# Performance work log

Measured on AMD Instinct MI355X. Metric: run time of the kernel, lower is better.

## Reference

```python
import jax, jax.numpy as jnp
import numpy as np

N_EMBD = 384
N_HEADS = 6
HEAD_SIZE = N_EMBD // N_HEADS  # 64
D_FF = 4 * N_EMBD
EPS = 1e-5


def layernorm(x, g, b):
    mu = jnp.mean(x, axis=-1, keepdims=True)
    var = jnp.var(x, axis=-1, keepdims=True)
    return (x - mu) * jax.lax.rsqrt(var + EPS) * g + b


def setup_inputs() -> dict:
    key = jax.random.key(0)
    ks = jax.random.split(key, 12)
    B, T, C, H, HS = 64, 256, N_EMBD, N_HEADS, HEAD_SIZE
    s = 0.02
    return {
        "x": jax.random.normal(ks[0], (B, T, C), jnp.float32),
        "Wq": jax.random.normal(ks[1], (H, C, HS), jnp.float32) * s,
        "Wk": jax.random.normal(ks[2], (H, C, HS), jnp.float32) * s,
        "Wv": jax.random.normal(ks[3], (H, C, HS), jnp.float32) * s,
        "Wo": jax.random.normal(ks[4], (C, C), jnp.float32) * s,
        "bo": jnp.zeros((C,), jnp.float32),
        "W1": jax.random.normal(ks[5], (C, D_FF), jnp.float32) * s,
        "b1": jnp.zeros((D_FF,), jnp.float32),
        "W2": jax.random.normal(ks[6], (D_FF, C), jnp.float32) * s,
        "b2": jnp.zeros((C,), jnp.float32),
        "g1": jnp.ones((C,), jnp.float32),
        "beta1": jnp.zeros((C,), jnp.float32),
        "g2": jnp.ones((C,), jnp.float32),
        "beta2": jnp.zeros((C,), jnp.float32),
    }


def reference(x, Wq, Wk, Wv, Wo, bo, W1, b1, W2, b2, g1, beta1, g2, beta2):
    B, T, C = x.shape
    # --- attention branch (dropout = identity in eval) ---
    h = layernorm(x, g1, beta1)
    q = jnp.einsum('btc,hck->bhtk', h, Wq)
    k = jnp.einsum('btc,hck->bhtk', h, Wk)
    v = jnp.einsum('btc,hck->bhtk', h, Wv)
    scale = HEAD_SIZE ** -0.5
    wei = jnp.einsum('bhtk,bhsk->bhts', q, k) * scale  # [B,H,T,T]
    causal = jnp.tril(jnp.ones((T, T), bool))
    wei = jnp.where(causal, wei, -jnp.inf)
    wei = jax.nn.softmax(wei, axis=-1)
    attn = jnp.einsum('bhts,bhsk->bthk', wei, v).reshape(B, T, C)
    x = x + attn @ Wo + bo
    # --- MLP branch ---
    h2 = layernorm(x, g2, beta2)
    ff = jax.nn.relu(h2 @ W1 + b1) @ W2 + b2
    return x + ff
```

## Files before the change

kernel.cpp:

```cpp
#include <hip/hip_runtime.h>

#define B 64
#define T 256
#define C 384
#define H 6
#define HS 64
#define DFF 1536
#define BT (B*T)

typedef __attribute__((ext_vector_type(8))) short short8;
typedef __attribute__((ext_vector_type(4))) float float4v;
typedef __attribute__((ext_vector_type(4))) unsigned short ushort4v;

static __device__ __forceinline__ unsigned short f2bf(float f) {
  unsigned int u = __float_as_uint(f);
  unsigned int r = (u + 0x7fffu + ((u >> 16) & 1u)) >> 16;
  return (unsigned short)r;
}

typedef __attribute__((address_space(1))) const unsigned int ga_u32;
typedef __attribute__((address_space(3))) unsigned int ls_u32;
static __device__ __forceinline__ void gld16(const void* g, void* l) {
  __builtin_amdgcn_global_load_lds((ga_u32*)g, (ls_u32*)l, 16, 0, 0);
}

__global__ __launch_bounds__(256) void prep_w(
    const float* __restrict__ Wq, const float* __restrict__ Wk, const float* __restrict__ Wv,
    const float* __restrict__ Wo, const float* __restrict__ W1, const float* __restrict__ W2,
    unsigned short* __restrict__ wqkv, unsigned short* __restrict__ wo,
    unsigned short* __restrict__ w1t, unsigned short* __restrict__ w2t) {
  __shared__ float tile[32][33];
  int bx = blockIdx.x;
  int x = threadIdx.x & 31, y = threadIdx.x >> 5;
  if (bx < 432) {
    int tn = bx % 36, tc = bx / 36;
    int n0 = tn * 32, c0 = tc * 32;
    int mat = n0 / 384, rem = n0 % 384, head = rem / 64, hs0 = rem % 64;
    const float* W = (mat == 0) ? Wq : ((mat == 1) ? Wk : Wv);
    const float* src = W + (size_t)head * C * HS + hs0;
    #pragma unroll
    for (int i = 0; i < 4; ++i) tile[y + 8 * i][x] = src[(size_t)(c0 + y + 8 * i) * 64 + x];
    __syncthreads();
    #pragma unroll
    for (int i = 0; i < 4; ++i)
      wqkv[(size_t)(n0 + y + 8 * i) * 384 + c0 + x] = f2bf(tile[x][y + 8 * i]);
    return;
  }
  const float* src; unsigned short* dst; int CN, R, n0, c0;
  if (bx < 576) {
    int t = bx - 432; n0 = (t % 12) * 32; c0 = (t / 12) * 32;
    src = Wo; dst = wo; CN = 384; R = 384;
  } else if (bx < 1152) {
    int t = bx - 576; n0 = (t % 48) * 32; c0 = (t / 48) * 32;
    src = W1; dst = w1t; CN = 1536; R = 384;
  } else {
    int t = bx - 1152; n0 = (t % 12) * 32; c0 = (t / 12) * 32;
    src = W2; dst = w2t; CN = 384; R = 1536;
  }
  #pragma unroll
  for (int i = 0; i < 4; ++i) tile[y + 8 * i][x] = src[(size_t)(c0 + y + 8 * i) * CN + n0 + x];
  __syncthreads();
  #pragma unroll
  for (int i = 0; i < 4; ++i)
    dst[(size_t)(n0 + y + 8 * i) * R + c0 + x] = f2bf(tile[x][y + 8 * i]);
}

__global__ __launch_bounds__(256) void ln_kernel(const float* __restrict__ x,
    const float* __restrict__ g, const float* __restrict__ bta,
    unsigned short* __restrict__ out) {
  int t = blockIdx.x * 4 + (threadIdx.x >> 6);
  int lane = threadIdx.x & 63;
  const float* row = x + (size_t)t * C;
  float v[6];
  float s = 0.f, ss = 0.f;
  #pragma unroll
  for (int i = 0; i < 6; ++i) {
    v[i] = row[lane + i * 64];
    s += v[i];
    ss += v[i] * v[i];
  }
  #pragma unroll
  for (int m = 32; m >= 1; m >>= 1) {
    s += __shfl_xor(s, m);
    ss += __shfl_xor(ss, m);
  }
  float mu = s / C;
  float var = ss / C - mu * mu;
  float rstd = rsqrtf(var + 1e-5f);
  unsigned short* orow = out + (size_t)t * C;
  #pragma unroll
  for (int i = 0; i < 6; ++i) {
    int c = lane + i * 64;
    orow[c] = f2bf((v[i] - mu) * rstd * g[c] + bta[c]);
  }
}

template<int EPI, int MT>
__global__ __launch_bounds__(MT >= 256 ? 512 : 256) void gemm_kernel(
    const unsigned short* __restrict__ A, const unsigned short* __restrict__ Wt,
    const float* __restrict__ bias, const float* __restrict__ resid,
    float* __restrict__ outf,
    unsigned short* __restrict__ outb, unsigned short* __restrict__ outb2,
    unsigned short* __restrict__ outb3, int K, int N) {
  __shared__ unsigned short Ash[MT * 64];
  __shared__ unsigned short Bsh[128 * 64];
  constexpr int NW = (MT >= 256) ? 8 : 4;
  constexpr int WM = NW / 2;
  constexpr int MR = MT / WM / 16;
  constexpr int NA = (MT / 8) / NW;
  constexpr int NB = 16 / NW;
  int tid = threadIdx.x, lane = tid & 63, w = tid >> 6;
  int wm = w >> 1, wn = w & 1;
  int bxs = ((blockIdx.x & 7) * (gridDim.x >> 3)) + (blockIdx.x >> 3);
  int m0 = bxs * MT, n0 = blockIdx.y * 128;
  int lrow = lane >> 3;
  int lchunk = (lane & 7) ^ (lrow & 7);
  int frow = lane & 15, cg = lane >> 4;
  float4v acc[MR][4] = {};
  for (int k0 = 0; k0 < K; k0 += 64) {
    __syncthreads();
    #pragma unroll
    for (int i = 0; i < NA; ++i) {
      int win = w * NA + i;
      gld16(A + (size_t)(m0 + win * 8 + lrow) * K + k0 + lchunk * 8, &Ash[win * 512]);
    }
    #pragma unroll
    for (int i = 0; i < NB; ++i) {
      int win = w * NB + i;
      gld16(Wt + (size_t)(n0 + win * 8 + lrow) * K + k0 + lchunk * 8, &Bsh[win * 512]);
    }
    __syncthreads();
    #pragma unroll
    for (int ks = 0; ks < 2; ++ks) {
      short8 af[MR], bf[4];
      #pragma unroll
      for (int mi = 0; mi < MR; ++mi) {
        int r = wm * (MR * 16) + mi * 16 + frow;
        int ch = (ks * 4 + cg) ^ (r & 7);
        af[mi] = *(const short8*)((const char*)Ash + r * 128 + ch * 16);
      }
      #pragma unroll
      for (int ni = 0; ni < 4; ++ni) {
        int r = wn * 64 + ni * 16 + frow;
        int ch = (ks * 4 + cg) ^ (r & 7);
        bf[ni] = *(const short8*)((const char*)Bsh + r * 128 + ch * 16);
      }
      #pragma unroll
      for (int mi = 0; mi < MR; ++mi)
        #pragma unroll
        for (int ni = 0; ni < 4; ++ni)
          acc[mi][ni] = __builtin_amdgcn_mfma_f32_16x16x32_bf16(af[mi], bf[ni], acc[mi][ni], 0, 0, 0);
    }
  }
  int cl = lane & 15;
  #pragma unroll
  for (int mi = 0; mi < MR; ++mi) {
    #pragma unroll
    for (int ni = 0; ni < 4; ++ni) {
      if constexpr (EPI == 0) {
        int gc = n0 + wn * 64 + ni * 16 + cl;
        int mat = gc / 384;
        int head = (gc % 384) >> 6;
        int hs = gc & 63;
        int gr0 = m0 + wm * (MR * 16) + mi * 16 + cg * 4;
        int tt0 = gr0 & 255, bidx = gr0 >> 8;
        size_t bhb = (size_t)(bidx * H + head);
        if (mat == 2) {
          ushort4v pk;
          #pragma unroll
          for (int j = 0; j < 4; ++j) pk[j] = f2bf(acc[mi][ni][j]);
          *(ushort4v*)&outb3[(bhb * HS + hs) * T + tt0] = pk;
        } else {
          unsigned short* dst = (mat == 0) ? outb : outb2;
          #pragma unroll
          for (int j = 0; j < 4; ++j)
            dst[(bhb * T + tt0 + j) * HS + hs] = f2bf(acc[mi][ni][j]);
        }
      } else {
        #pragma unroll
        for (int j = 0; j < 4; ++j) {
          int gr = m0 + wm * (MR * 16) + mi * 16 + cg * 4 + j;
          int gc = n0 + wn * 64 + ni * 16 + cl;
          float val = acc[mi][ni][j];
          if constexpr (EPI == 2) {
            outb[(size_t)gr * N + gc] = f2bf(fmaxf(val + bias[gc], 0.f));
          } else {
            size_t i = (size_t)gr * N + gc;
            outf[i] = resid[i] + val + bias[gc];
          }
        }
      }
    }
  }
}

__global__ __launch_bounds__(512) void proj_ln_kernel(
    const unsigned short* __restrict__ A, const unsigned short* __restrict__ Wt,
    const float* __restrict__ bo, const float* __restrict__ x,
    const float* __restrict__ g2, const float* __restrict__ be2,
    float* __restrict__ x2, unsigned short* __restrict__ h2) {
  __shared__ unsigned short Ash[64 * 64];
  __shared__ unsigned short Bsh[384 * 64];
  __shared__ float red[64][2][2];
  int tid = threadIdx.x, lane = tid & 63, w = tid >> 6;
  int wm = w >> 1, wn = w & 1;
  int bxs = ((blockIdx.x & 7) * (gridDim.x >> 3)) + (blockIdx.x >> 3);
  int m0 = bxs * 64;
  int lrow = lane >> 3;
  int lchunk = (lane & 7) ^ (lrow & 7);
  int frow = lane & 15, cg = lane >> 4, cl = lane & 15;
  float4v acc[12] = {};
  for (int k0 = 0; k0 < 384; k0 += 64) {
    __syncthreads();
    gld16(A + (size_t)(m0 + w * 8 + lrow) * 384 + k0 + lchunk * 8, &Ash[w * 512]);
    #pragma unroll
    for (int i = 0; i < 6; ++i) {
      int win = w * 6 + i;
      gld16(Wt + (size_t)(win * 8 + lrow) * 384 + k0 + lchunk * 8, &Bsh[win * 512]);
    }
    __syncthreads();
    #pragma unroll
    for (int ks = 0; ks < 2; ++ks) {
      int ra = wm * 16 + frow;
      int cha = (ks * 4 + cg) ^ (ra & 7);
      short8 af = *(const short8*)((const char*)Ash + ra * 128 + cha * 16);
      #pragma unroll
      for (int nt = 0; nt < 12; ++nt) {
        int rb = wn * 192 + nt * 16 + frow;
        int chb = (ks * 4 + cg) ^ (rb & 7);
        short8 bf = *(const short8*)((const char*)Bsh + rb * 128 + chb * 16);
        acc[nt] = __builtin_amdgcn_mfma_f32_16x16x32_bf16(af, bf, acc[nt], 0, 0, 0);
      }
    }
  }
  #pragma unroll
  for (int nt = 0; nt < 12; ++nt) {
    int gc = wn * 192 + nt * 16 + cl;
    #pragma unroll
    for (int j = 0; j < 4; ++j) {
      int gr = m0 + wm * 16 + cg * 4 + j;
      acc[nt][j] += x[(size_t)gr * 384 + gc] + bo[gc];
    }
  }
  __syncthreads();
  #pragma unroll
  for (int j = 0; j < 4; ++j) {
    float s = 0.f, ss = 0.f;
    #pragma unroll
    for (int nt = 0; nt < 12; ++nt) { float v = acc[nt][j]; s += v; ss += v * v; }
    #pragma unroll
    for (int off = 1; off < 16; off <<= 1) { s += __shfl_xor(s, off); ss += __shfl_xor(ss, off); }
    if (cl == 0) {
      int lr = wm * 16 + cg * 4 + j;
      red[lr][wn][0] = s;
      red[lr][wn][1] = ss;
    }
  }
  __syncthreads();
  #pragma unroll
  for (int j = 0; j < 4; ++j) {
    int lr = wm * 16 + cg * 4 + j;
    int gr = m0 + lr;
    float s = red[lr][0][0] + red[lr][1][0];
    float ss = red[lr][0][1] + red[lr][1][1];
    float mu = s / 384.f;
    float var = ss / 384.f - mu * mu;
    float rstd = rsqrtf(var + 1e-5f);
    #pragma unroll
    for (int nt = 0; nt < 12; ++nt) {
      int gc = wn * 192 + nt * 16 + cl;
      float v = acc[nt][j];
      x2[(size_t)gr * 384 + gc] = v;
      h2[(size_t)gr * 384 + gc] = f2bf((v - mu) * rstd * g2[gc] + be2[gc]);
    }
  }
}

__global__ __launch_bounds__(256) void attn_kernel(
    const unsigned short* __restrict__ qg, const unsigned short* __restrict__ kg,
    const unsigned short* __restrict__ vtg, unsigned short* __restrict__ ab) {
  __shared__ unsigned short Ksh[64 * 64];
  __shared__ unsigned short Vsh[64 * 256];
  __shared__ unsigned short Psh[4 * 16 * 256];
  int bh = blockIdx.x;
  int bb = bh / H, hh = bh % H;
  int qt = blockIdx.y, q0 = qt * 64;
  int tid = threadIdx.x, lane = tid & 63, w = tid >> 6;
  int cl = lane & 15, cg = lane >> 4;
  const float scale_log2e = 0.125f * 1.44269504f;
  const unsigned short* qp = qg + ((size_t)bh * T) * HS;
  const unsigned short* kp = kg + ((size_t)bh * T) * HS;
  const unsigned short* vp = vtg + ((size_t)bh * HS) * T;

  short8 aq[2];
  #pragma unroll
  for (int k0 = 0; k0 < 2; ++k0)
    aq[k0] = *(const short8*)&qp[(size_t)(q0 + w * 16 + cl) * HS + cg * 8 + k0 * 32];

  #pragma unroll
  for (int i = 0; i < 8; ++i) {
    int idx = tid + i * 256;
    int r = idx >> 5, c16 = idx & 31;
    uint4 val = *(const uint4*)&vp[(size_t)r * T + c16 * 8];
    int byte = (r * 512 + c16 * 16) ^ ((r & 7) << 4);
    *(uint4*)((char*)Vsh + byte) = val;
  }

  float4v sacc[4][4] = {};
  for (int si = 0; si <= qt; ++si) {
    __syncthreads();
    #pragma unroll
    for (int i = 0; i < 2; ++i) {
      int idx = tid + i * 256;
      int r = idx >> 3, c16 = idx & 7;
      uint4 val = *(const uint4*)&kp[(size_t)(si * 64 + r) * HS + c16 * 8];
      int byte = (r * 128 + c16 * 16) ^ ((r & 7) << 4);
      *(uint4*)((char*)Ksh + byte) = val;
    }
    __syncthreads();
    #pragma unroll
    for (int ss = 0; ss < 4; ++ss) {
      if (ss == si) {
        #pragma unroll
        for (int nt = 0; nt < 4; ++nt) {
          int srow = nt * 16 + cl;
          #pragma unroll
          for (int k0 = 0; k0 < 2; ++k0) {
            int byte = (srow * 128 + (cg * 8 + k0 * 32) * 2) ^ ((srow & 7) << 4);
            short8 bf = *(const short8*)((char*)Ksh + byte);
            sacc[ss][nt] = __builtin_amdgcn_mfma_f32_16x16x32_bf16(aq[k0], bf, sacc[ss][nt], 0, 0, 0);
          }
        }
      }
    }
  }

  #pragma unroll
  for (int si = 0; si < 4; ++si) {
    if (si == qt) {
      #pragma unroll
      for (int nt = 0; nt < 4; ++nt) {
        int s = q0 + nt * 16 + cl;
        #pragma unroll
        for (int j = 0; j < 4; ++j) {
          int q = q0 + w * 16 + cg * 4 + j;
          if (s > q) sacc[si][nt][j] = -1e30f;
        }
      }
    }
  }

  float lj[4];
  #pragma unroll
  for (int j = 0; j < 4; ++j) {
    float m = -1e30f;
    #pragma unroll
    for (int si = 0; si < 4; ++si) if (si <= qt)
      #pragma unroll
      for (int nt = 0; nt < 4; ++nt) m = fmaxf(m, sacc[si][nt][j]);
    #pragma unroll
    for (int off = 1; off < 16; off <<= 1) m = fmaxf(m, __shfl_xor(m, off));
    float l = 0.f;
    #pragma unroll
    for (int si = 0; si < 4; ++si) if (si <= qt)
      #pragma unroll
      for (int nt = 0; nt < 4; ++nt) {
        float p0 = exp2f((sacc[si][nt][j] - m) * scale_log2e);
        sacc[si][nt][j] = p0;
        l += p0;
      }
    #pragma unroll
    for (int off = 1; off < 16; off <<= 1) l += __shfl_xor(l, off);
    lj[j] = 1.f / l;
  }

  char* pbase = (char*)Psh + w * 8192;
  #pragma unroll
  for (int si = 0; si < 4; ++si) if (si <= qt)
    #pragma unroll
    for (int nt = 0; nt < 4; ++nt)
      #pragma unroll
      for (int j = 0; j < 4; ++j) {
        int prow = cg * 4 + j, col = si * 64 + nt * 16 + cl;
        int byte = (prow * 512 + col * 2) ^ ((prow & 7) << 4);
        *(unsigned short*)(pbase + byte) = f2bf(sacc[si][nt][j]);
      }

  int nks = 2 * (qt + 1);
  #pragma unroll
  for (int nt = 0; nt < 4; ++nt) {
    float4v oacc = {};
    for (int ks = 0; ks < nks; ++ks) {
      int k = ks * 32 + cg * 8;
      int pbyte = (cl * 512 + k * 2) ^ ((cl & 7) << 4);
      short8 af = *(const short8*)(pbase + pbyte);
      int vr = nt * 16 + cl;
      int vbyte = (vr * 512 + k * 2) ^ ((vr & 7) << 4);
      short8 bf = *(const short8*)((char*)Vsh + vbyte);
      oacc = __builtin_amdgcn_mfma_f32_16x16x32_bf16(af, bf, oacc, 0, 0, 0);
    }
    #pragma unroll
    for (int j = 0; j < 4; ++j) {
      int t = q0 + w * 16 + cg * 4 + j;
      ab[((size_t)(bb * T + t)) * C + hh * 64 + nt * 16 + cl] = f2bf(oacc[j] * lj[j]);
    }
  }
}

extern "C" void kernel_launch(void* const* d_in, const int* in_sizes, int n_in,
                              void* d_out, int out_size, void* d_ws, size_t ws_size,
                              hipStream_t stream) {
  const float* x   = (const float*)d_in[0];
  const float* Wq  = (const float*)d_in[1];
  const float* Wk  = (const float*)d_in[2];
  const float* Wv  = (const float*)d_in[3];
  const float* Wo  = (const float*)d_in[4];
  const float* bo  = (const float*)d_in[5];
  const float* W1  = (const float*)d_in[6];
  const float* b1  = (const float*)d_in[7];
  const float* W2  = (const float*)d_in[8];
  const float* b2  = (const float*)d_in[9];
  const float* g1  = (const float*)d_in[10];
  const float* be1 = (const float*)d_in[11];
  const float* g2  = (const float*)d_in[12];
  const float* be2 = (const float*)d_in[13];
  float* out = (float*)d_out;
  float* ws = (float*)d_ws;

  unsigned short* wqkv_t = (unsigned short*)ws;
  unsigned short* wo_t   = wqkv_t + 442368;
  unsigned short* w1t    = wo_t + 147456;
  unsigned short* w2t    = w1t + 589824;
  float* base2 = ws + 884736;
  unsigned short* h  = (unsigned short*)base2;
  float* x2 = base2 + 3145728;
  unsigned short* ab = (unsigned short*)(x2 + 6291456);
  unsigned short* qb = (unsigned short*)(x2 + 6291456 + 3145728);
  unsigned short* kb = qb + 6291456;
  unsigned short* vt = kb + 6291456;
  unsigned short* ffb = ab;

  prep_w<<<1728, 256, 0, stream>>>(Wq, Wk, Wv, Wo, W1, W2, wqkv_t, wo_t, w1t, w2t);
  ln_kernel<<<BT / 4, 256, 0, stream>>>(x, g1, be1, h);
  gemm_kernel<0, 256><<<dim3(64, 9), 512, 0, stream>>>(h, wqkv_t, nullptr, nullptr,
                                                       nullptr, qb, kb, vt, 384, 1152);
  attn_kernel<<<dim3(B * H, T / 64), 256, 0, stream>>>(qb, kb, vt, ab);
  proj_ln_kernel<<<256, 512, 0, stream>>>(ab, wo_t, bo, x, g2, be2, x2, h);
  gemm_kernel<2, 256><<<dim3(64, 12), 512, 0, stream>>>(h, w1t, b1, nullptr,
                                                        nullptr, ffb, nullptr, nullptr, 384, 1536);
  gemm_kernel<3, 64><<<dim3(256, 3), 256, 0, stream>>>(ffb, w2t, b2, x2,
                                                       out, nullptr, nullptr, nullptr, 1536, 384);
}
```

Baseline: 151.7 us.

## Double-buffer LDS tiles in FFN2 GEMM and K tiles in attention

Adds an optional double-buffered LDS path to the GEMM kernel, enabled only for the FFN down-projection (K=1536), so the next k-tile's global-to-LDS load is issued before computing on the current one. This removes one barrier per iteration. The attention kernel also double-buffers K tiles, prefetching the next tile into registers during the QK MFMAs. The cost is doubled LDS use for these kernels, which may lower occupancy, plus extra registers for the prefetch.

After: 153.9 us. Within noise of the previous version (+1.4%).

```diff
diff --git a/kernel.cpp b/kernel.cpp
--- a/kernel.cpp
+++ b/kernel.cpp
@@ -95,15 +95,15 @@
   }
 }
 
-template<int EPI, int MT>
+template<int EPI, int MT, bool DB>
 __global__ __launch_bounds__(MT >= 256 ? 512 : 256) void gemm_kernel(
     const unsigned short* __restrict__ A, const unsigned short* __restrict__ Wt,
     const float* __restrict__ bias, const float* __restrict__ resid,
     float* __restrict__ outf,
     unsigned short* __restrict__ outb, unsigned short* __restrict__ outb2,
     unsigned short* __restrict__ outb3, int K, int N) {
-  __shared__ unsigned short Ash[MT * 64];
-  __shared__ unsigned short Bsh[128 * 64];
+  __shared__ unsigned short Ash[(DB ? 2 : 1) * MT * 64];
+  __shared__ unsigned short Bsh[(DB ? 2 : 1) * 128 * 64];
   constexpr int NW = (MT >= 256) ? 8 : 4;
   constexpr int WM = NW / 2;
   constexpr int MR = MT / WM / 16;
@@ -117,19 +117,24 @@
   int lchunk = (lane & 7) ^ (lrow & 7);
   int frow = lane & 15, cg = lane >> 4;
   float4v acc[MR][4] = {};
-  for (int k0 = 0; k0 < K; k0 += 64) {
-    __syncthreads();
+
+  auto STAGE = [&](int b, int k0) {
     #pragma unroll
     for (int i = 0; i < NA; ++i) {
       int win = w * NA + i;
-      gld16(A + (size_t)(m0 + win * 8 + lrow) * K + k0 + lchunk * 8, &Ash[win * 512]);
+      gld16(A + (size_t)(m0 + win * 8 + lrow) * K + k0 + lchunk * 8,
+            &Ash[b * MT * 64 + win * 512]);
     }
     #pragma unroll
     for (int i = 0; i < NB; ++i) {
       int win = w * NB + i;
-      gld16(Wt + (size_t)(n0 + win * 8 + lrow) * K + k0 + lchunk * 8, &Bsh[win * 512]);
-    }
-    __syncthreads();
+      gld16(Wt + (size_t)(n0 + win * 8 + lrow) * K + k0 + lchunk * 8,
+            &Bsh[b * 128 * 64 + win * 512]);
+    }
+  };
+  auto COMPUTE = [&](int b) {
+    const char* Ab = (const char*)&Ash[b * MT * 64];
+    const char* Bb = (const char*)&Bsh[b * 128 * 64];
     #pragma unroll
     for (int ks = 0; ks < 2; ++ks) {
       short8 af[MR], bf[4];
@@ -137,13 +142,13 @@
       for (int mi = 0; mi < MR; ++mi) {
         int r = wm * (MR * 16) + mi * 16 + frow;
         int ch = (ks * 4 + cg) ^ (r & 7);
-        af[mi] = *(const short8*)((const char*)Ash + r * 128 + ch * 16);
+        af[mi] = *(const short8*)(Ab + r * 128 + ch * 16);
       }
       #pragma unroll
       for (int ni = 0; ni < 4; ++ni) {
         int r = wn * 64 + ni * 16 + frow;
         int ch = (ks * 4 + cg) ^ (r & 7);
-        bf[ni] = *(const short8*)((const char*)Bsh + r * 128 + ch * 16);
+        bf[ni] = *(const short8*)(Bb + r * 128 + ch * 16);
       }
       #pragma unroll
       for (int mi = 0; mi < MR; ++mi)
@@ -151,7 +156,27 @@
         for (int ni = 0; ni < 4; ++ni)
           acc[mi][ni] = __builtin_amdgcn_mfma_f32_16x16x32_bf16(af[mi], bf[ni], acc[mi][ni], 0, 0, 0);
     }
-  }
+  };
+
+  if constexpr (DB) {
+    STAGE(0, 0);
+    __syncthreads();
+    int ntile = K / 64, buf = 0;
+    for (int t = 0; t < ntile; ++t) {
+      if (t + 1 < ntile) STAGE(buf ^ 1, (t + 1) * 64);
+      COMPUTE(buf);
+      __syncthreads();
+      buf ^= 1;
+    }
+  } else {
+    for (int k0 = 0; k0 < K; k0 += 64) {
+      __syncthreads();
+      STAGE(0, k0);
+      __syncthreads();
+      COMPUTE(0);
+    }
+  }
+
   int cl = lane & 15;
   #pragma unroll
   for (int mi = 0; mi < MR; ++mi) {
@@ -279,7 +304,7 @@
 __global__ __launch_bounds__(256) void attn_kernel(
     const unsigned short* __restrict__ qg, const unsigned short* __restrict__ kg,
     const unsigned short* __restrict__ vtg, unsigned short* __restrict__ ab) {
-  __shared__ unsigned short Ksh[64 * 64];
+  __shared__ unsigned short Ksh[2][64 * 64];
   __shared__ unsigned short Vsh[64 * 256];
   __shared__ unsigned short Psh[4 * 16 * 256];
   int bh = blockIdx.x;
@@ -306,18 +331,35 @@
     *(uint4*)((char*)Vsh + byte) = val;
   }
 
-  float4v sacc[4][4] = {};
-  for (int si = 0; si <= qt; ++si) {
-    __syncthreads();
+  auto loadK = [&](int si, uint4 v[2]) {
     #pragma unroll
     for (int i = 0; i < 2; ++i) {
       int idx = tid + i * 256;
       int r = idx >> 3, c16 = idx & 7;
-      uint4 val = *(const uint4*)&kp[(size_t)(si * 64 + r) * HS + c16 * 8];
+      v[i] = *(const uint4*)&kp[(size_t)(si * 64 + r) * HS + c16 * 8];
+    }
+  };
+  auto writeK = [&](int b, uint4 v[2]) {
+    #pragma unroll
+    for (int i = 0; i < 2; ++i) {
+      int idx = tid + i * 256;
+      int r = idx >> 3, c16 = idx & 7;
       int byte = (r * 128 + c16 * 16) ^ ((r & 7) << 4);
-      *(uint4*)((char*)Ksh + byte) = val;
-    }
-    __syncthreads();
+      *(uint4*)((char*)Ksh[b] + byte) = v[i];
+    }
+  };
+
+  float4v sacc[4][4] = {};
+  {
+    uint4 kv[2];
+    loadK(0, kv);
+    writeK(0, kv);
+  }
+  __syncthreads();
+  int buf = 0;
+  for (int si = 0; si <= qt; ++si) {
+    uint4 kn[2];
+    if (si < qt) loadK(si + 1, kn);
     #pragma unroll
     for (int ss = 0; ss < 4; ++ss) {
       if (ss == si) {
@@ -327,12 +369,15 @@
           #pragma unroll
           for (int k0 = 0; k0 < 2; ++k0) {
             int byte = (srow * 128 + (cg * 8 + k0 * 32) * 2) ^ ((srow & 7) << 4);
-            short8 bf = *(const short8*)((char*)Ksh + byte);
+            short8 bf = *(const short8*)((char*)Ksh[buf] + byte);
             sacc[ss][nt] = __builtin_amdgcn_mfma_f32_16x16x32_bf16(aq[k0], bf, sacc[ss][nt], 0, 0, 0);
           }
         }
       }
     }
+    if (si < qt) writeK(buf ^ 1, kn);
+    __syncthreads();
+    buf ^= 1;
   }
 
   #pragma unroll
@@ -442,12 +487,12 @@
 
   prep_w<<<1728, 256, 0, stream>>>(Wq, Wk, Wv, Wo, W1, W2, wqkv_t, wo_t, w1t, w2t);
   ln_kernel<<<BT / 4, 256, 0, stream>>>(x, g1, be1, h);
-  gemm_kernel<0, 256><<<dim3(64, 9), 512, 0, stream>>>(h, wqkv_t, nullptr, nullptr,
-                                                       nullptr, qb, kb, vt, 384, 1152);
+  gemm_kernel<0, 256, false><<<dim3(64, 9), 512, 0, stream>>>(h, wqkv_t, nullptr, nullptr,
+                                                              nullptr, qb, kb, vt, 384, 1152);
   attn_kernel<<<dim3(B * H, T / 64), 256, 0, stream>>>(qb, kb, vt, ab);
   proj_ln_kernel<<<256, 512, 0, stream>>>(ab, wo_t, bo, x, g2, be2, x2, h);
-  gemm_kernel<2, 256><<<dim3(64, 12), 512, 0, stream>>>(h, w1t, b1, nullptr,
-                                                        nullptr, ffb, nullptr, nullptr, 384, 1536);
-  gemm_kernel<3, 64><<<dim3(256, 3), 256, 0, stream>>>(ffb, w2t, b2, x2,
-                                                       out, nullptr, nullptr, nullptr, 1536, 384);
-}
+  gemm_kernel<2, 256, false><<<dim3(64, 12), 512, 0, stream>>>(h, w1t, b1, nullptr,
+                                                               nullptr, ffb, nullptr, nullptr, 384, 1536);
+  gemm_kernel<3, 64, true><<<dim3(256, 3), 256, 0, stream>>>(ffb, w2t, b2, x2,
+                                                             out, nullptr, nullptr, nullptr, 1536, 384);
+}
```
